# Kernel optimization log

Measured on AMD Instinct MI355X. Metric: run time of the kernel, lower is better.

Reference implementation:

```python
import jax, jax.numpy as jnp
import numpy as np

N_NODES = 50000
IN_DIM = 128
HIDDEN = 64
OUT_DIM = 3
HEADS1 = 4
NEG_SLOPE = 0.2
EPS = 1e-16


def _glorot(key, shape):
    fan_in, fan_out = shape[0], shape[-1]
    lim = (6.0 / (fan_in + fan_out)) ** 0.5
    return jax.random.uniform(key, shape, jnp.float32, -lim, lim)


def setup_inputs() -> dict:
    key = jax.random.key(0)
    ks = jax.random.split(key, 12)
    x = jax.random.normal(ks[0], (N_NODES, IN_DIM), jnp.float32)
    edge_index = jax.random.randint(ks[1], (2, 400000), 0, N_NODES, jnp.int64)
    # layer 1: GATConv(in=128, out=64, heads=4)
    W1 = _glorot(ks[2], (IN_DIM, HEADS1 * HIDDEN))
    att_src1 = _glorot(ks[3], (HEADS1, HIDDEN))
    att_dst1 = _glorot(ks[4], (HEADS1, HIDDEN))
    b1 = jnp.zeros((HEADS1 * HIDDEN,), jnp.float32)
    # layer 2: GATConv(in=256, out=64, heads=1)
    W2 = _glorot(ks[5], (HEADS1 * HIDDEN, HIDDEN))
    att_src2 = _glorot(ks[6], (1, HIDDEN))
    att_dst2 = _glorot(ks[7], (1, HIDDEN))
    b2 = jnp.zeros((HIDDEN,), jnp.float32)
    # output linear
    Wout = _glorot(ks[8], (HIDDEN, OUT_DIM))
    bout = jnp.zeros((OUT_DIM,), jnp.float32)
    return {"x": x, "edge_index": edge_index, "W1": W1, "att_src1": att_src1,
            "att_dst1": att_dst1, "b1": b1, "W2": W2, "att_src2": att_src2,
            "att_dst2": att_dst2, "b2": b2, "Wout": Wout, "bout": bout}


def gat_conv(x, src, dst, W, a_src, a_dst, b, n_nodes):
    H, C = a_src.shape
    h = (x @ W).reshape(n_nodes, H, C)            # [N,H,C]
    a_s = jnp.sum(h * a_src[None], axis=-1)        # [N,H]
    a_d = jnp.sum(h * a_dst[None], axis=-1)        # [N,H]
    e = jax.nn.leaky_relu(a_s[src] + a_d[dst], NEG_SLOPE)  # [E,H]
    # segment softmax over incoming edges of each dst node
    m = jax.ops.segment_max(e, dst, num_segments=n_nodes)
    ex = jnp.exp(e - m[dst])
    denom = jax.ops.segment_sum(ex, dst, num_segments=n_nodes)
    alpha = ex / (denom[dst] + EPS)                # [E,H]
    msg = h[src] * alpha[..., None]                # [E,H,C]
    out = jax.ops.segment_sum(msg, dst, num_segments=n_nodes)
    return out.reshape(n_nodes, H * C) + b


def reference(x, edge_index, W1, att_src1, att_dst1, b1, W2, att_src2, att_dst2, b2, Wout, bout):
    n = x.shape[0]
    loop = jnp.arange(n, dtype=edge_index.dtype)
    src = jnp.concatenate([edge_index[0], loop])   # add self loops (PyG default)
    dst = jnp.concatenate([edge_index[1], loop])
    h = gat_conv(x, src, dst, W1, att_src1, att_dst1, b1, n)
    h = jax.nn.elu(h)
    h = gat_conv(h, src, dst, W2, att_src2, att_dst2, b2, n)
    h = jax.nn.elu(h)
    return h @ Wout + bout
```

## Files before the change

kernel.cpp:

```cpp
#include <hip/hip_runtime.h>
#include <hip/hip_bf16.h>
#include <math.h>

#define N_NODES  50000
#define IN_DIM   128
#define HIDDEN   64
#define OUT_DIM  3
#define HEADS1   4
#define E_RAW    400000
#define E_TOT    450000
#define NEG_SLOPE 0.2f
#define SCAN_CHUNK 1024
#define N_CHUNKS ((N_NODES + SCAN_CHUNK - 1) / SCAN_CHUNK)
#define WPREP_BLOCKS 128

typedef __attribute__((ext_vector_type(8))) short bf16x8;
typedef __attribute__((ext_vector_type(4))) float f32x4;

static __device__ __forceinline__ float bfu(unsigned short u) {
    return __uint_as_float(((unsigned)u) << 16);
}
static __device__ __forceinline__ unsigned short f2b_bits(float v) {
    __hip_bfloat16 b = __float2bfloat16(v);
    return *reinterpret_cast<unsigned short*>(&b);
}

static __device__ __forceinline__ void get_edge(const int* __restrict__ ei, int is64,
                                                int e, int& s, int& d) {
    if (e >= E_RAW) { s = d = e - E_RAW; return; }
    if (is64) { s = ei[2 * e]; d = ei[2 * E_RAW + 2 * e]; }
    else      { s = ei[e];     d = ei[E_RAW + e]; }
    s = min(max(s, 0), N_NODES - 1);
    d = min(max(d, 0), N_NODES - 1);
}

__global__ void detect_int64_kernel(const int* __restrict__ ei, int* __restrict__ flag) {
    __shared__ int any_nonzero;
    if (threadIdx.x == 0) any_nonzero = 0;
    __syncthreads();
    for (int i = threadIdx.x; i < 8192; i += blockDim.x) {
        int k = i * 48;
        if (ei[2 * k + 1] != 0) any_nonzero = 1;
    }
    __syncthreads();
    if (threadIdx.x == 0) flag[0] = (any_nonzero == 0) ? 1 : 0;
}

__global__ void wprep_count_kernel(const float* __restrict__ W1, __hip_bfloat16* __restrict__ W1T,
                                   const float* __restrict__ W2, __hip_bfloat16* __restrict__ W2T,
                                   const int* __restrict__ ei, const int* __restrict__ flag,
                                   int* __restrict__ deg) {
    int bid = blockIdx.x;
    if (bid < WPREP_BLOCKS) {
        int i = bid * 256 + threadIdx.x;
        if (i < 256 * 128) {
            int n = i >> 7, k = i & 127;
            *((unsigned short*)W1T + i) = f2b_bits(W1[k * 256 + n]);
        }
        if (i < 64 * 256) {
            int n = i >> 8, k = i & 255;
            *((unsigned short*)W2T + i) = f2b_bits(W2[k * 64 + n]);
        }
        return;
    }
    int e = (bid - WPREP_BLOCKS) * 256 + threadIdx.x;
    if (e >= E_TOT) return;
    int s, d;
    get_edge(ei, flag[0], e, s, d);
    atomicAdd(&deg[d], 1);
}

__global__ void scan_local_kernel(const int* __restrict__ deg, int* __restrict__ row_ptr,
                                  int* __restrict__ bsums) {
    __shared__ int buf[SCAN_CHUNK];
    int base = blockIdx.x * SCAN_CHUNK;
    int i = base + threadIdx.x;
    buf[threadIdx.x] = (i < N_NODES) ? deg[i] : 0;
    __syncthreads();
    for (int off = 1; off < SCAN_CHUNK; off <<= 1) {
        int t = (threadIdx.x >= off) ? buf[threadIdx.x - off] : 0;
        __syncthreads();
        buf[threadIdx.x] += t;
        __syncthreads();
    }
    if (i < N_NODES) row_ptr[i + 1] = buf[threadIdx.x];
    if (threadIdx.x == SCAN_CHUNK - 1) bsums[blockIdx.x] = buf[SCAN_CHUNK - 1];
    if (blockIdx.x == 0 && threadIdx.x == 0) row_ptr[0] = 0;
}

__global__ void scan_bsums_kernel(int* __restrict__ bsums) {
    __shared__ int buf[64];
    int i = threadIdx.x;
    buf[i] = (i < N_CHUNKS) ? bsums[i] : 0;
    __syncthreads();
    for (int off = 1; off < 64; off <<= 1) {
        int t = (i >= off) ? buf[i - off] : 0;
        __syncthreads();
        buf[i] += t;
        __syncthreads();
    }
    if (i < N_CHUNKS) bsums[i] = (i == 0) ? 0 : buf[i - 1];
}

__global__ void scan_add_kernel(int* __restrict__ row_ptr, const int* __restrict__ bsums,
                                const int* __restrict__ deg, int* __restrict__ cursor) {
    int i = blockIdx.x * blockDim.x + threadIdx.x;
    if (i < N_NODES) {
        int incl = row_ptr[i + 1] + bsums[i / SCAN_CHUNK];
        row_ptr[i + 1] = incl;
        cursor[i] = incl - deg[i];
    }
}

__global__ void scatter_kernel(const int* __restrict__ ei, const int* __restrict__ flag,
                               int* __restrict__ cursor, int* __restrict__ csr_src) {
    int e = blockIdx.x * blockDim.x + threadIdx.x;
    if (e >= E_TOT) return;
    int s, d;
    get_edge(ei, flag[0], e, s, d);
    int pos = atomicAdd(&cursor[d], 1);
    csr_src[pos] = s;
}

__global__ void __launch_bounds__(256) gemm_l1_mfma_kernel(
        const float* __restrict__ x, const __hip_bfloat16* __restrict__ W1T,
        const float* __restrict__ att_s, const float* __restrict__ att_d,
        __hip_bfloat16* __restrict__ h1,
        float* __restrict__ asb4, float* __restrict__ adb4) {
    __shared__ unsigned short As[16][136];
    const int tid = threadIdx.x;
    const int wave = tid >> 6, lane = tid & 63;
    const int quad = lane >> 4, m = lane & 15;
    const int row0 = blockIdx.x * 16;
    {
        int r = tid >> 4, seg = tid & 15;
        const float* xa = x + (size_t)(row0 + r) * IN_DIM + seg * 8;
        float4 u = *(const float4*)xa;
        float4 v = *(const float4*)(xa + 4);
        ushort4 p0, p1;
        p0.x = f2b_bits(u.x); p0.y = f2b_bits(u.y); p0.z = f2b_bits(u.z); p0.w = f2b_bits(u.w);
        p1.x = f2b_bits(v.x); p1.y = f2b_bits(v.y); p1.z = f2b_bits(v.z); p1.w = f2b_bits(v.w);
        *(ushort4*)&As[r][seg * 8]     = p0;
        *(ushort4*)&As[r][seg * 8 + 4] = p1;
    }
    __syncthreads();
    const int n0w = wave * 64;
    f32x4 acc0 = {0.f, 0.f, 0.f, 0.f}, acc1 = acc0, acc2 = acc0, acc3 = acc0;
    #pragma unroll
    for (int k0 = 0; k0 < IN_DIM; k0 += 32) {
        int kk = k0 + quad * 8;
        bf16x8 a = *(const bf16x8*)&As[m][kk];
        bf16x8 b0 = *(const bf16x8*)(W1T + (size_t)(n0w +  0 + m) * IN_DIM + kk);
        bf16x8 b1 = *(const bf16x8*)(W1T + (size_t)(n0w + 16 + m) * IN_DIM + kk);
        bf16x8 b2 = *(const bf16x8*)(W1T + (size_t)(n0w + 32 + m) * IN_DIM + kk);
        bf16x8 b3 = *(const bf16x8*)(W1T + (size_t)(n0w + 48 + m) * IN_DIM + kk);
        acc0 = __builtin_amdgcn_mfma_f32_16x16x32_bf16(a, b0, acc0, 0, 0, 0);
        acc1 = __builtin_amdgcn_mfma_f32_16x16x32_bf16(a, b1, acc1, 0, 0, 0);
        acc2 = __builtin_amdgcn_mfma_f32_16x16x32_bf16(a, b2, acc2, 0, 0, 0);
        acc3 = __builtin_amdgcn_mfma_f32_16x16x32_bf16(a, b3, acc3, 0, 0, 0);
    }
    float ats0 = att_s[n0w +  0 + m], atd0 = att_d[n0w +  0 + m];
    float ats1 = att_s[n0w + 16 + m], atd1 = att_d[n0w + 16 + m];
    float ats2 = att_s[n0w + 32 + m], atd2 = att_d[n0w + 32 + m];
    float ats3 = att_s[n0w + 48 + m], atd3 = att_d[n0w + 48 + m];
    unsigned short* out = (unsigned short*)h1;
    #pragma unroll
    for (int i = 0; i < 4; i++) {
        int grow = row0 + quad * 4 + i;
        size_t base = (size_t)grow * 256;
        out[base + n0w +  0 + m] = f2b_bits(acc0[i]);
        out[base + n0w + 16 + m] = f2b_bits(acc1[i]);
        out[base + n0w + 32 + m] = f2b_bits(acc2[i]);
        out[base + n0w + 48 + m] = f2b_bits(acc3[i]);
        float ps = acc0[i] * ats0 + acc1[i] * ats1 + acc2[i] * ats2 + acc3[i] * ats3;
        float pd = acc0[i] * atd0 + acc1[i] * atd1 + acc2[i] * atd2 + acc3[i] * atd3;
        #pragma unroll
        for (int off = 1; off < 16; off <<= 1) {
            ps += __shfl_xor(ps, off, 16);
            pd += __shfl_xor(pd, off, 16);
        }
        if (m == 0) {
            asb4[grow * 4 + wave] = ps;
            adb4[grow * 4 + wave] = pd;
        }
    }
}

__global__ void __launch_bounds__(256) gemm_l2_mfma_kernel(
        const __hip_bfloat16* __restrict__ eluagg, const __hip_bfloat16* __restrict__ W2T,
        const float* __restrict__ att_s, const float* __restrict__ att_d,
        __hip_bfloat16* __restrict__ h2,
        float* __restrict__ asb, float* __restrict__ adb) {
    __shared__ float sPS[4][16];
    __shared__ float sPD[4][16];
    const int tid = threadIdx.x;
    const int wave = tid >> 6, lane = tid & 63;
    const int quad = lane >> 4, m = lane & 15;
    const int row0 = blockIdx.x * 16;
    const int n0 = wave * 16;
    f32x4 acc = {0.f, 0.f, 0.f, 0.f};
    #pragma unroll
    for (int k0 = 0; k0 < 256; k0 += 32) {
        int kk = k0 + quad * 8;
        bf16x8 a = *(const bf16x8*)(eluagg + (size_t)(row0 + m) * 256 + kk);
        bf16x8 b = *(const bf16x8*)(W2T + (size_t)(n0 + m) * 256 + kk);
        acc = __builtin_amdgcn_mfma_f32_16x16x32_bf16(a, b, acc, 0, 0, 0);
    }
    float ats = att_s[n0 + m], atd = att_d[n0 + m];
    unsigned short* out = (unsigned short*)h2;
    #pragma unroll
    for (int i = 0; i < 4; i++) {
        int grow = row0 + quad * 4 + i;
        out[(size_t)grow * 64 + n0 + m] = f2b_bits(acc[i]);
        float ps = acc[i] * ats;
        float pd = acc[i] * atd;
        #pragma unroll
        for (int off = 1; off < 16; off <<= 1) {
            ps += __shfl_xor(ps, off, 16);
            pd += __shfl_xor(pd, off, 16);
        }
        if (m == 0) {
            sPS[wave][quad * 4 + i] = ps;
            sPD[wave][quad * 4 + i] = pd;
        }
    }
    __syncthreads();
    if (tid < 16) {
        float ps = sPS[0][tid] + sPS[1][tid] + sPS[2][tid] + sPS[3][tid];
        float pd = sPD[0][tid] + sPD[1][tid] + sPD[2][tid] + sPD[3][tid];
        asb[row0 + tid] = ps;
        adb[row0 + tid] = pd;
    }
}

__global__ void __launch_bounds__(256) gat_gather4_kernel(
        const int* __restrict__ row_ptr, const int* __restrict__ csr_src,
        const float* __restrict__ asb4, const float* __restrict__ adb4,
        const __hip_bfloat16* __restrict__ h1, const float* __restrict__ bias,
        __hip_bfloat16* __restrict__ eluagg) {
    int wave = threadIdx.x >> 6;
    int lane = threadIdx.x & 63;
    int n = blockIdx.x * 4 + wave;
    if (n >= N_NODES) return;
    int b = row_ptr[n], e = row_ptr[n + 1];
    int head = lane >> 4;
    float adn = adb4[n * 4 + head];
    float4 a0 = make_float4(0, 0, 0, 0), a1 = a0, a2 = a0, a3 = a0;
    float l0 = 0.f, l1 = 0.f, l2 = 0.f, l3 = 0.f;
    int j = b;
    for (; j + 4 <= e; j += 4) {
        int s0 = csr_src[j], s1 = csr_src[j + 1], s2 = csr_src[j + 2], s3 = csr_src[j + 3];
        float v0 = asb4[s0 * 4 + head] + adn;
        float v1 = asb4[s1 * 4 + head] + adn;
        float v2 = asb4[s2 * 4 + head] + adn;
        float v3 = asb4[s3 * 4 + head] + adn;
        v0 = (v0 > 0.f) ? v0 : NEG_SLOPE * v0;
        v1 = (v1 > 0.f) ? v1 : NEG_SLOPE * v1;
        v2 = (v2 > 0.f) ? v2 : NEG_SLOPE * v2;
        v3 = (v3 > 0.f) ? v3 : NEG_SLOPE * v3;
        float w0 = __expf(v0), w1 = __expf(v1), w2 = __expf(v2), w3 = __expf(v3);
        ushort4 f0 = *(const ushort4*)(h1 + (size_t)s0 * 256 + lane * 4);
        ushort4 f1 = *(const ushort4*)(h1 + (size_t)s1 * 256 + lane * 4);
        ushort4 f2 = *(const ushort4*)(h1 + (size_t)s2 * 256 + lane * 4);
        ushort4 f3 = *(const ushort4*)(h1 + (size_t)s3 * 256 + lane * 4);
        l0 += w0; l1 += w1; l2 += w2; l3 += w3;
        a0.x += w0 * bfu(f0.x); a0.y += w0 * bfu(f0.y); a0.z += w0 * bfu(f0.z); a0.w += w0 * bfu(f0.w);
        a1.x += w1 * bfu(f1.x); a1.y += w1 * bfu(f1.y); a1.z += w1 * bfu(f1.z); a1.w += w1 * bfu(f1.w);
        a2.x += w2 * bfu(f2.x); a2.y += w2 * bfu(f2.y); a2.z += w2 * bfu(f2.z); a2.w += w2 * bfu(f2.w);
        a3.x += w3 * bfu(f3.x); a3.y += w3 * bfu(f3.y); a3.z += w3 * bfu(f3.z); a3.w += w3 * bfu(f3.w);
    }
    for (; j < e; j++) {
        int s = csr_src[j];
        float v = asb4[s * 4 + head] + adn;
        v = (v > 0.f) ? v : NEG_SLOPE * v;
        float w = __expf(v);
        ushort4 f = *(const ushort4*)(h1 + (size_t)s * 256 + lane * 4);
        l0 += w;
        a0.x += w * bfu(f.x); a0.y += w * bfu(f.y); a0.z += w * bfu(f.z); a0.w += w * bfu(f.w);
    }
    float il = 1.f / ((l0 + l1) + (l2 + l3) + 1e-16f);
    float4 bb = *(const float4*)(bias + lane * 4);
    float4 r;
    r.x = (a0.x + a1.x + a2.x + a3.x) * il + bb.x;
    r.y = (a0.y + a1.y + a2.y + a3.y) * il + bb.y;
    r.z = (a0.z + a1.z + a2.z + a3.z) * il + bb.z;
    r.w = (a0.w + a1.w + a2.w + a3.w) * il + bb.w;
    r.x = (r.x > 0.f) ? r.x : expm1f(r.x);
    r.y = (r.y > 0.f) ? r.y : expm1f(r.y);
    r.z = (r.z > 0.f) ? r.z : expm1f(r.z);
    r.w = (r.w > 0.f) ? r.w : expm1f(r.w);
    ushort4 st;
    st.x = f2b_bits(r.x); st.y = f2b_bits(r.y); st.z = f2b_bits(r.z); st.w = f2b_bits(r.w);
    *(ushort4*)(eluagg + (size_t)n * 256 + lane * 4) = st;
}

__global__ void __launch_bounds__(256) gat_gather1_out_kernel(
        const int* __restrict__ row_ptr, const int* __restrict__ csr_src,
        const float* __restrict__ asb, const float* __restrict__ adb,
        const __hip_bfloat16* __restrict__ h2, const float* __restrict__ bias,
        const float* __restrict__ Wout, const float* __restrict__ bout,
        float* __restrict__ out) {
    int wave = threadIdx.x >> 6;
    int lane = threadIdx.x & 63;
    int n = blockIdx.x * 4 + wave;
    if (n >= N_NODES) return;
    int b = row_ptr[n], e = row_ptr[n + 1];
    int cg = lane & 15, slot = lane >> 4;
    float adn = adb[n];
    float4 acc = make_float4(0, 0, 0, 0);
    float l = 0.f;
    for (int j0 = b; j0 < e; j0 += 4) {
        int j = j0 + slot;
        float w = 0.f; int s = 0;
        if (j < e) {
            s = csr_src[j];
            float v = asb[s] + adn;
            v = (v > 0.f) ? v : NEG_SLOPE * v;
            w = __expf(v);
        }
        ushort4 f = *(const ushort4*)(h2 + (size_t)s * 64 + cg * 4);
        l += w;
        acc.x += w * bfu(f.x); acc.y += w * bfu(f.y);
        acc.z += w * bfu(f.z); acc.w += w * bfu(f.w);
    }
    acc.x += __shfl_xor(acc.x, 16, 64); acc.y += __shfl_xor(acc.y, 16, 64);
    acc.z += __shfl_xor(acc.z, 16, 64); acc.w += __shfl_xor(acc.w, 16, 64);
    l += __shfl_xor(l, 16, 64);
    acc.x += __shfl_xor(acc.x, 32, 64); acc.y += __shfl_xor(acc.y, 32, 64);
    acc.z += __shfl_xor(acc.z, 32, 64); acc.w += __shfl_xor(acc.w, 32, 64);
    l += __shfl_xor(l, 32, 64);
    float il = 1.f / (l + 1e-16f);
    float4 bb = *(const float4*)(bias + cg * 4);
    float4 v;
    v.x = acc.x * il + bb.x; v.y = acc.y * il + bb.y;
    v.z = acc.z * il + bb.z; v.w = acc.w * il + bb.w;
    v.x = (v.x > 0.f) ? v.x : expm1f(v.x);
    v.y = (v.y > 0.f) ? v.y : expm1f(v.y);
    v.z = (v.z > 0.f) ? v.z : expm1f(v.z);
    v.w = (v.w > 0.f) ? v.w : expm1f(v.w);
    int c0 = cg * 4;
    float o0 = v.x * Wout[(c0+0)*OUT_DIM+0] + v.y * Wout[(c0+1)*OUT_DIM+0]
             + v.z * Wout[(c0+2)*OUT_DIM+0] + v.w * Wout[(c0+3)*OUT_DIM+0];
    float o1 = v.x * Wout[(c0+0)*OUT_DIM+1] + v.y * Wout[(c0+1)*OUT_DIM+1]
             + v.z * Wout[(c0+2)*OUT_DIM+1] + v.w * Wout[(c0+3)*OUT_DIM+1];
    float o2 = v.x * Wout[(c0+0)*OUT_DIM+2] + v.y * Wout[(c0+1)*OUT_DIM+2]
             + v.z * Wout[(c0+2)*OUT_DIM+2] + v.w * Wout[(c0+3)*OUT_DIM+2];
    #pragma unroll
    for (int off = 1; off < 16; off <<= 1) {
        o0 += __shfl_xor(o0, off, 64);
        o1 += __shfl_xor(o1, off, 64);
        o2 += __shfl_xor(o2, off, 64);
    }
    if (lane == 0) {
        out[n * OUT_DIM + 0] = o0 + bout[0];
        out[n * OUT_DIM + 1] = o1 + bout[1];
        out[n * OUT_DIM + 2] = o2 + bout[2];
    }
}

extern "C" void kernel_launch(void* const* d_in, const int* in_sizes, int n_in,
                              void* d_out, int out_size, void* d_ws, size_t ws_size,
                              hipStream_t stream) {
    const float* x    = (const float*)d_in[0];
    const int*   ei   = (const int*)d_in[1];
    const float* W1   = (const float*)d_in[2];
    const float* as1  = (const float*)d_in[3];
    const float* ad1  = (const float*)d_in[4];
    const float* b1   = (const float*)d_in[5];
    const float* W2   = (const float*)d_in[6];
    const float* as2  = (const float*)d_in[7];
    const float* ad2  = (const float*)d_in[8];
    const float* b2v  = (const float*)d_in[9];
    const float* Wout = (const float*)d_in[10];
    const float* bout = (const float*)d_in[11];
    float* out = (float*)d_out;

    float* ws    = (float*)d_ws;
    int*   flag  = (int*)ws;
    float* asb4  = ws + 16;
    float* adb4  = asb4 + (size_t)N_NODES * 4;
    float* asb1  = adb4 + (size_t)N_NODES * 4;
    float* adb1  = asb1 + N_NODES;
    __hip_bfloat16* h1     = (__hip_bfloat16*)(adb1 + N_NODES);
    __hip_bfloat16* eluagg = (__hip_bfloat16*)(h1 + (size_t)N_NODES * 256);
    __hip_bfloat16* h2     = (__hip_bfloat16*)(eluagg + (size_t)N_NODES * 256);
    __hip_bfloat16* W1T    = (__hip_bfloat16*)(h2 + (size_t)N_NODES * 64);
    __hip_bfloat16* W2T    = W1T + 256 * 128;
    int* deg     = (int*)(W2T + 64 * 256);
    int* bsums   = deg + N_NODES;
    int* row_ptr = bsums + 64;
    int* cursor  = row_ptr + N_NODES + 16;
    int* csr_src = cursor + N_NODES;

    const int EB = (E_TOT + 255) / 256;
    const int NB = (N_NODES + 255) / 256;
    const int AB = (N_NODES + 3) / 4;
    const int MB = N_NODES / 16;

    detect_int64_kernel<<<1, 256, 0, stream>>>(ei, flag);
    hipMemsetAsync(deg, 0, (size_t)N_NODES * sizeof(int), stream);

    wprep_count_kernel<<<WPREP_BLOCKS + EB, 256, 0, stream>>>(W1, W1T, W2, W2T, ei, flag, deg);
    scan_local_kernel<<<N_CHUNKS, SCAN_CHUNK, 0, stream>>>(deg, row_ptr, bsums);
    scan_bsums_kernel<<<1, 64, 0, stream>>>(bsums);
    scan_add_kernel<<<NB, 256, 0, stream>>>(row_ptr, bsums, deg, cursor);
    scatter_kernel<<<EB, 256, 0, stream>>>(ei, flag, cursor, csr_src);

    gemm_l1_mfma_kernel<<<MB, 256, 0, stream>>>(x, W1T, as1, ad1, h1, asb4, adb4);
    gat_gather4_kernel<<<AB, 256, 0, stream>>>(row_ptr, csr_src, asb4, adb4, h1, b1, eluagg);

    gemm_l2_mfma_kernel<<<MB, 256, 0, stream>>>(eluagg, W2T, as2, ad2, h2, asb1, adb1);
    gat_gather1_out_kernel<<<AB, 256, 0, stream>>>(row_ptr, csr_src, asb1, adb1, h2,
                                                   b2v, Wout, bout, out);
}
```

Measured before the change: 282.9 us.

## Restructure GAT gather kernels with cooperative edge-index loads and 16-byte feature loads

Both aggregation kernels now load a chunk of edge source indices cooperatively, one per lane, and compute attention weights in parallel across lanes. Each edge's index and weight is then broadcast with shuffles. Feature rows are read as 16-byte bf16x8 vectors, with each half (layer 1) or each eighth (layer 2) of the wave handling a different edge, and partial sums are reduced with xor-shuffles. This aims to cut redundant scalar index and attention loads and serialized exp work, and to widen memory transactions. In exchange it adds shuffle traffic, and in layer 1 only half the lanes are active for the epilogue store.

```diff
diff --git a/kernel.cpp b/kernel.cpp
--- a/kernel.cpp
+++ b/kernel.cpp
@@ -243,55 +243,58 @@
     int n = blockIdx.x * 4 + wave;
     if (n >= N_NODES) return;
     int b = row_ptr[n], e = row_ptr[n + 1];
-    int head = lane >> 4;
-    float adn = adb4[n * 4 + head];
-    float4 a0 = make_float4(0, 0, 0, 0), a1 = a0, a2 = a0, a3 = a0;
-    float l0 = 0.f, l1 = 0.f, l2 = 0.f, l3 = 0.f;
-    int j = b;
-    for (; j + 4 <= e; j += 4) {
-        int s0 = csr_src[j], s1 = csr_src[j + 1], s2 = csr_src[j + 2], s3 = csr_src[j + 3];
-        float v0 = asb4[s0 * 4 + head] + adn;
-        float v1 = asb4[s1 * 4 + head] + adn;
-        float v2 = asb4[s2 * 4 + head] + adn;
-        float v3 = asb4[s3 * 4 + head] + adn;
-        v0 = (v0 > 0.f) ? v0 : NEG_SLOPE * v0;
-        v1 = (v1 > 0.f) ? v1 : NEG_SLOPE * v1;
-        v2 = (v2 > 0.f) ? v2 : NEG_SLOPE * v2;
-        v3 = (v3 > 0.f) ? v3 : NEG_SLOPE * v3;
-        float w0 = __expf(v0), w1 = __expf(v1), w2 = __expf(v2), w3 = __expf(v3);
-        ushort4 f0 = *(const ushort4*)(h1 + (size_t)s0 * 256 + lane * 4);
-        ushort4 f1 = *(const ushort4*)(h1 + (size_t)s1 * 256 + lane * 4);
-        ushort4 f2 = *(const ushort4*)(h1 + (size_t)s2 * 256 + lane * 4);
-        ushort4 f3 = *(const ushort4*)(h1 + (size_t)s3 * 256 + lane * 4);
-        l0 += w0; l1 += w1; l2 += w2; l3 += w3;
-        a0.x += w0 * bfu(f0.x); a0.y += w0 * bfu(f0.y); a0.z += w0 * bfu(f0.z); a0.w += w0 * bfu(f0.w);
-        a1.x += w1 * bfu(f1.x); a1.y += w1 * bfu(f1.y); a1.z += w1 * bfu(f1.z); a1.w += w1 * bfu(f1.w);
-        a2.x += w2 * bfu(f2.x); a2.y += w2 * bfu(f2.y); a2.z += w2 * bfu(f2.z); a2.w += w2 * bfu(f2.w);
-        a3.x += w3 * bfu(f3.x); a3.y += w3 * bfu(f3.y); a3.z += w3 * bfu(f3.z); a3.w += w3 * bfu(f3.w);
-    }
-    for (; j < e; j++) {
-        int s = csr_src[j];
-        float v = asb4[s * 4 + head] + adn;
-        v = (v > 0.f) ? v : NEG_SLOPE * v;
-        float w = __expf(v);
-        ushort4 f = *(const ushort4*)(h1 + (size_t)s * 256 + lane * 4);
-        l0 += w;
-        a0.x += w * bfu(f.x); a0.y += w * bfu(f.y); a0.z += w * bfu(f.z); a0.w += w * bfu(f.w);
-    }
-    float il = 1.f / ((l0 + l1) + (l2 + l3) + 1e-16f);
-    float4 bb = *(const float4*)(bias + lane * 4);
-    float4 r;
-    r.x = (a0.x + a1.x + a2.x + a3.x) * il + bb.x;
-    r.y = (a0.y + a1.y + a2.y + a3.y) * il + bb.y;
-    r.z = (a0.z + a1.z + a2.z + a3.z) * il + bb.z;
-    r.w = (a0.w + a1.w + a2.w + a3.w) * il + bb.w;
-    r.x = (r.x > 0.f) ? r.x : expm1f(r.x);
-    r.y = (r.y > 0.f) ? r.y : expm1f(r.y);
-    r.z = (r.z > 0.f) ? r.z : expm1f(r.z);
-    r.w = (r.w > 0.f) ? r.w : expm1f(r.w);
-    ushort4 st;
-    st.x = f2b_bits(r.x); st.y = f2b_bits(r.y); st.z = f2b_bits(r.z); st.w = f2b_bits(r.w);
-    *(ushort4*)(eluagg + (size_t)n * 256 + lane * 4) = st;
+    const int c    = lane & 31;
+    const int slot = lane >> 5;
+    const int head = c >> 3;
+    const int ei   = lane >> 2;
+    const int hh   = lane & 3;
+    float adnh = adb4[n * 4 + hh];
+    float acc[8];
+    #pragma unroll
+    for (int i = 0; i < 8; i++) acc[i] = 0.f;
+    float l = 0.f;
+    for (int c0 = b; c0 < e; c0 += 16) {
+        int cnt = min(16, e - c0);
+        int s_all = (lane < cnt) ? csr_src[c0 + lane] : 0;
+        int sE = __shfl(s_all, ei, 64);
+        float w_all = 0.f;
+        if (ei < cnt) {
+            float v = asb4[sE * 4 + hh] + adnh;
+            v = (v > 0.f) ? v : NEG_SLOPE * v;
+            w_all = __expf(v);
+        }
+        #pragma unroll 2
+        for (int k = 0; k < cnt; k += 2) {
+            int eidx = k + slot;
+            int s = __shfl(s_all, eidx, 64);
+            float w = __shfl(w_all, eidx * 4 + head, 64);
+            bf16x8 f = *(const bf16x8*)(h1 + (size_t)s * 256 + c * 8);
+            l += w;
+            #pragma unroll
+            for (int i = 0; i < 8; i++)
+                acc[i] += w * bfu((unsigned short)f[i]);
+        }
+    }
+    #pragma unroll
+    for (int i = 0; i < 8; i++) acc[i] += __shfl_xor(acc[i], 32, 64);
+    l += __shfl_xor(l, 32, 64);
+    if (lane < 32) {
+        float il = 1.f / (l + 1e-16f);
+        float4 b0 = *(const float4*)(bias + c * 8);
+        float4 b1 = *(const float4*)(bias + c * 8 + 4);
+        float r[8];
+        r[0] = acc[0] * il + b0.x; r[1] = acc[1] * il + b0.y;
+        r[2] = acc[2] * il + b0.z; r[3] = acc[3] * il + b0.w;
+        r[4] = acc[4] * il + b1.x; r[5] = acc[5] * il + b1.y;
+        r[6] = acc[6] * il + b1.z; r[7] = acc[7] * il + b1.w;
+        bf16x8 st;
+        #pragma unroll
+        for (int i = 0; i < 8; i++) {
+            float v = (r[i] > 0.f) ? r[i] : expm1f(r[i]);
+            st[i] = (short)f2b_bits(v);
+        }
+        *(bf16x8*)(eluagg + (size_t)n * 256 + c * 8) = st;
+    }
 }
 
 __global__ void __launch_bounds__(256) gat_gather1_out_kernel(
@@ -305,48 +308,60 @@
     int n = blockIdx.x * 4 + wave;
     if (n >= N_NODES) return;
     int b = row_ptr[n], e = row_ptr[n + 1];
-    int cg = lane & 15, slot = lane >> 4;
+    const int c    = lane & 7;
+    const int slot = lane >> 3;
     float adn = adb[n];
-    float4 acc = make_float4(0, 0, 0, 0);
+    float acc[8];
+    #pragma unroll
+    for (int i = 0; i < 8; i++) acc[i] = 0.f;
     float l = 0.f;
-    for (int j0 = b; j0 < e; j0 += 4) {
-        int j = j0 + slot;
-        float w = 0.f; int s = 0;
-        if (j < e) {
-            s = csr_src[j];
-            float v = asb[s] + adn;
+    for (int c0 = b; c0 < e; c0 += 64) {
+        int cnt = min(64, e - c0);
+        int s_all = (lane < cnt) ? csr_src[c0 + lane] : 0;
+        float w_all = 0.f;
+        if (lane < cnt) {
+            float v = asb[s_all] + adn;
             v = (v > 0.f) ? v : NEG_SLOPE * v;
-            w = __expf(v);
-        }
-        ushort4 f = *(const ushort4*)(h2 + (size_t)s * 64 + cg * 4);
-        l += w;
-        acc.x += w * bfu(f.x); acc.y += w * bfu(f.y);
-        acc.z += w * bfu(f.z); acc.w += w * bfu(f.w);
-    }
-    acc.x += __shfl_xor(acc.x, 16, 64); acc.y += __shfl_xor(acc.y, 16, 64);
-    acc.z += __shfl_xor(acc.z, 16, 64); acc.w += __shfl_xor(acc.w, 16, 64);
-    l += __shfl_xor(l, 16, 64);
-    acc.x += __shfl_xor(acc.x, 32, 64); acc.y += __shfl_xor(acc.y, 32, 64);
-    acc.z += __shfl_xor(acc.z, 32, 64); acc.w += __shfl_xor(acc.w, 32, 64);
-    l += __shfl_xor(l, 32, 64);
+            w_all = __expf(v);
+        }
+        #pragma unroll 2
+        for (int k = 0; k < cnt; k += 8) {
+            int eidx = k + slot;
+            int s = __shfl(s_all, eidx, 64);
+            float w = __shfl(w_all, eidx, 64);
+            bf16x8 f = *(const bf16x8*)(h2 + (size_t)s * 64 + c * 8);
+            l += w;
+            #pragma unroll
+            for (int i = 0; i < 8; i++)
+                acc[i] += w * bfu((unsigned short)f[i]);
+        }
+    }
+    #pragma unroll
+    for (int off = 8; off < 64; off <<= 1) {
+        #pragma unroll
+        for (int i = 0; i < 8; i++) acc[i] += __shfl_xor(acc[i], off, 64);
+        l += __shfl_xor(l, off, 64);
+    }
     float il = 1.f / (l + 1e-16f);
-    float4 bb = *(const float4*)(bias + cg * 4);
-    float4 v;
-    v.x = acc.x * il + bb.x; v.y = acc.y * il + bb.y;
-    v.z = acc.z * il + bb.z; v.w = acc.w * il + bb.w;
-    v.x = (v.x > 0.f) ? v.x : expm1f(v.x);
-    v.y = (v.y > 0.f) ? v.y : expm1f(v.y);
-    v.z = (v.z > 0.f) ? v.z : expm1f(v.z);
-    v.w = (v.w > 0.f) ? v.w : expm1f(v.w);
-    int c0 = cg * 4;
-    float o0 = v.x * Wout[(c0+0)*OUT_DIM+0] + v.y * Wout[(c0+1)*OUT_DIM+0]
-             + v.z * Wout[(c0+2)*OUT_DIM+0] + v.w * Wout[(c0+3)*OUT_DIM+0];
-    float o1 = v.x * Wout[(c0+0)*OUT_DIM+1] + v.y * Wout[(c0+1)*OUT_DIM+1]
-             + v.z * Wout[(c0+2)*OUT_DIM+1] + v.w * Wout[(c0+3)*OUT_DIM+1];
-    float o2 = v.x * Wout[(c0+0)*OUT_DIM+2] + v.y * Wout[(c0+1)*OUT_DIM+2]
-             + v.z * Wout[(c0+2)*OUT_DIM+2] + v.w * Wout[(c0+3)*OUT_DIM+2];
-    #pragma unroll
-    for (int off = 1; off < 16; off <<= 1) {
+    float4 b0 = *(const float4*)(bias + c * 8);
+    float4 b1 = *(const float4*)(bias + c * 8 + 4);
+    float v[8];
+    v[0] = acc[0] * il + b0.x; v[1] = acc[1] * il + b0.y;
+    v[2] = acc[2] * il + b0.z; v[3] = acc[3] * il + b0.w;
+    v[4] = acc[4] * il + b1.x; v[5] = acc[5] * il + b1.y;
+    v[6] = acc[6] * il + b1.z; v[7] = acc[7] * il + b1.w;
+    #pragma unroll
+    for (int i = 0; i < 8; i++) v[i] = (v[i] > 0.f) ? v[i] : expm1f(v[i]);
+    const float* wp = Wout + c * 24;
+    float o0 = 0.f, o1 = 0.f, o2 = 0.f;
+    #pragma unroll
+    for (int i = 0; i < 8; i++) {
+        o0 += v[i] * wp[i * 3 + 0];
+        o1 += v[i] * wp[i * 3 + 1];
+        o2 += v[i] * wp[i * 3 + 2];
+    }
+    #pragma unroll
+    for (int off = 1; off < 8; off <<= 1) {
         o0 += __shfl_xor(o0, off, 64);
         o1 += __shfl_xor(o1, off, 64);
         o2 += __shfl_xor(o2, off, 64);
```

After: 284.9 us. About the same (+0.7%).
